# Optimization experiments

Measured on AMD Instinct MI355X. Metric: run time of the kernel, lower is better.

## Reference

```python
import jax, jax.numpy as jnp
import numpy as np

V, D, H, L, B, T = 32000, 1024, 1024, 4, 32, 128
PAD_ID = 0


def setup_inputs() -> dict:
    key = jax.random.key(0)
    ks = jax.random.split(key, 12)
    s = lambda fan: 1.0 / np.sqrt(fan)
    dec_input = jax.random.randint(ks[0], (B, T), 0, V)
    h0 = jax.random.normal(ks[1], (L, B, H), jnp.float32)
    c0 = jax.random.normal(ks[2], (L, B, H), jnp.float32)
    emb = jax.random.normal(ks[3], (V, D), jnp.float32) * 0.02
    emb = emb.at[PAD_ID].set(0.0)
    # all layers have input size H (layer0 input = embedding_dim = H)
    W_ih = jax.random.uniform(ks[4], (L, 4 * H, H), jnp.float32, -s(H), s(H))
    W_hh = jax.random.uniform(ks[5], (L, 4 * H, H), jnp.float32, -s(H), s(H))
    b_ih = jax.random.uniform(ks[6], (L, 4 * H), jnp.float32, -s(H), s(H))
    b_hh = jax.random.uniform(ks[7], (L, 4 * H), jnp.float32, -s(H), s(H))
    cls_W = jax.random.uniform(ks[8], (V, H), jnp.float32, -s(H), s(H))
    cls_b = jax.random.uniform(ks[9], (V,), jnp.float32, -s(H), s(H))
    return {"dec_input": dec_input, "h0": h0, "c0": c0, "emb": emb,
            "W_ih": W_ih, "W_hh": W_hh, "b_ih": b_ih, "b_hh": b_hh,
            "cls_W": cls_W, "cls_b": cls_b}


def _lstm_stack_step(carry, x_t, W_ih, W_hh, b_ih, b_hh):
    # carry: (h [L,B,H], c [L,B,H]); x_t: [B,H]
    h, c = carry
    inp = x_t
    hs, cs = [], []
    n_layers = W_ih.shape[0]
    for l in range(n_layers):
        gates = inp @ W_ih[l].T + h[l] @ W_hh[l].T + b_ih[l] + b_hh[l]
        i_g, f_g, g_g, o_g = jnp.split(gates, 4, axis=-1)
        c_new = jax.nn.sigmoid(f_g) * c[l] + jax.nn.sigmoid(i_g) * jnp.tanh(g_g)
        h_new = jax.nn.sigmoid(o_g) * jnp.tanh(c_new)
        inp = h_new + inp  # residual connection (dropout p=0)
        hs.append(h_new)
        cs.append(c_new)
    return (jnp.stack(hs, 0), jnp.stack(cs, 0)), inp


def reference(dec_input, h0, c0, emb, W_ih, W_hh, b_ih, b_hh, cls_W, cls_b):
    embedded = emb[dec_input]                 # [B,T,D]
    xs = jnp.swapaxes(embedded, 0, 1)         # [T,B,D]

    def step(carry, x_t):
        return _lstm_stack_step(carry, x_t, W_ih, W_hh, b_ih, b_hh)

    (hT, cT), outs = jax.lax.scan(step, (h0, c0), xs)  # outs: [T,B,H]
    outputs = jnp.swapaxes(outs, 0, 1)         # [B,T,H]
    logits = outputs @ cls_W.T + cls_b         # [B,T,V]
    return logits, (hT, cT)
```

## Files before the change

### kernel.cpp

```cpp
#include <hip/hip_runtime.h>
#include <stdint.h>

#define LAYERS 4
#define BATCH  32
#define SEQT   128
#define HID    1024
#define VOCAB  32000

typedef __attribute__((ext_vector_type(8))) short short8;
typedef __attribute__((ext_vector_type(8))) __bf16 bf16x8;
typedef __attribute__((ext_vector_type(4))) float floatx4;

#define CLS_OFF  0ul
#define X_OFF    65536000ul
#define RES_OFF  73924608ul
#define HBT_OFF  107479040ul
#define CF_OFF   141295616ul
#define SYNC_OFF 141819904ul

#define LOGITS_N 131072000ul
#define BH (BATCH * HID)

__device__ __forceinline__ unsigned short f2bf(float f) {
  union { float f; unsigned u; } v; v.f = f;
  unsigned r = v.u + 0x7FFF + ((v.u >> 16) & 1);
  return (unsigned short)(r >> 16);
}
__device__ __forceinline__ float bf2f(unsigned short b) {
  union { unsigned u; float f; } v; v.u = ((unsigned)b) << 16;
  return v.f;
}
__device__ __forceinline__ floatx4 mfma16(short8 a, short8 b, floatx4 c) {
  return __builtin_amdgcn_mfma_f32_16x16x32_bf16(
      __builtin_bit_cast(bf16x8, a), __builtin_bit_cast(bf16x8, b), c, 0, 0, 0);
}
__device__ __forceinline__ short8 cvt8(float4 a, float4 b) {
  short8 r;
  r[0] = (short)f2bf(a.x); r[1] = (short)f2bf(a.y);
  r[2] = (short)f2bf(a.z); r[3] = (short)f2bf(a.w);
  r[4] = (short)f2bf(b.x); r[5] = (short)f2bf(b.y);
  r[6] = (short)f2bf(b.z); r[7] = (short)f2bf(b.w);
  return r;
}


__global__ void k_convert(const float* __restrict__ clsw, unsigned short* __restrict__ oC) {
  const long long NC4 = 8192000LL;
  for (long long i = (long long)blockIdx.x * blockDim.x + threadIdx.x; i < NC4;
       i += (long long)gridDim.x * blockDim.x) {
    float4 v = *(const float4*)(clsw + (i << 2));
    ushort4 o; o.x = f2bf(v.x); o.y = f2bf(v.y); o.z = f2bf(v.z); o.w = f2bf(v.w);
    *(ushort4*)(oC + (i << 2)) = o;
  }
}

__global__ void k_embed(const int* __restrict__ tok, const float* __restrict__ emb,
                        unsigned short* __restrict__ X) {
  const int bt = blockIdx.x;
  const int t = bt >> 5, b = bt & 31;
  const int v = tok[b * SEQT + t];
  const float4* src = (const float4*)(emb + (size_t)v * HID);
  ushort4* dst = (ushort4*)(X + (size_t)bt * HID);
  const int i = threadIdx.x;
  float4 f = src[i];
  ushort4 o; o.x = f2bf(f.x); o.y = f2bf(f.y); o.z = f2bf(f.z); o.w = f2bf(f.w);
  dst[i] = o;
}

__global__ void k_init(const float* __restrict__ h0, const float* __restrict__ c0,
                       unsigned short* __restrict__ HBT, float* __restrict__ CF,
                       unsigned* __restrict__ sync) {
  const int i = blockIdx.x * blockDim.x + threadIdx.x;
  if (i < 4096) sync[i] = 0u;
  if (i < LAYERS * BATCH * HID) {
    HBT[i] = f2bf(h0[i]);
    CF[i] = c0[i];
  }
}


__global__ __launch_bounds__(512, 2) void k_lstm(
    const float* __restrict__ Wih, const float* __restrict__ Whh,
    const float* __restrict__ bih, const float* __restrict__ bhh,
    const unsigned short* __restrict__ X, unsigned short* __restrict__ RES,
    unsigned short* __restrict__ HBT, const float* __restrict__ CF,
    float* __restrict__ out, unsigned* __restrict__ syncp) {
  const int p = blockIdx.x;
  const int l = (p & 7) >> 1;
  const int jj = ((p >> 3) << 1) | (p & 1);
  const int j0 = jj << 4;
  const int tid = threadIdx.x;
  const int q = tid >> 6;
  const int lane = tid & 63;
  const int lo = lane & 15, hi = lane >> 4;
  const int u = tid & 15, b = tid >> 4;

  __shared__ float red[8][32][66];
  __shared__ unsigned mbx, mbh;

  if (tid == 0) { mbx = 0u; mbh = 0u; }

  (void)__hip_atomic_load(syncp + 2048, __ATOMIC_ACQUIRE, __HIP_MEMORY_SCOPE_AGENT);

  const unsigned* fx = syncp + (((l - 1) & 3) * 64 + lane) * 4;
  const unsigned* fh = syncp + (l * 64 + lane) * 4;
  unsigned* fown = syncp + (l * 64 + jj) * 4;

  short8 wx[4][4], wh[4][4];
  {
    const size_t lb = (size_t)l * 4096;
#pragma unroll
    for (int ct = 0; ct < 4; ++ct) {
#pragma unroll
      for (int ks = 0; ks < 4; ++ks) {
        const size_t off = (lb + (size_t)(ct * 1024 + j0 + lo)) * HID
                         + (size_t)q * 128 + ks * 32 + hi * 8;
        float4 a0 = *(const float4*)(Wih + off);
        float4 a1 = *(const float4*)(Wih + off + 4);
        wx[ct][ks] = cvt8(a0, a1);
        float4 b0 = *(const float4*)(Whh + off);
        float4 b1 = *(const float4*)(Whh + off + 4);
        wh[ct][ks] = cvt8(b0, b1);
      }
    }
  }
  float bias_g[4];
#pragma unroll
  for (int g = 0; g < 4; ++g)
    bias_g[g] = bih[l * 4096 + g * 1024 + j0 + u] + bhh[l * 4096 + g * 1024 + j0 + u];
  float c_reg = CF[(size_t)l * BH + (size_t)b * HID + j0 + u];

  __syncthreads();

  for (int t = 0; t < SEQT; ++t) {
    if (q == 0) {
      if (l > 0) {
        for (;;) {
          int ok = (__hip_atomic_load(fx, __ATOMIC_RELAXED, __HIP_MEMORY_SCOPE_AGENT)
                    >= (unsigned)(t + 1));
          if (__all(ok)) break;
          __builtin_amdgcn_s_sleep(1);
        }
      }
      __hip_atomic_store(&mbx, (unsigned)(t + 1),
                         __ATOMIC_RELAXED, __HIP_MEMORY_SCOPE_WORKGROUP);
    } else {
      while (__hip_atomic_load(&mbx, __ATOMIC_RELAXED, __HIP_MEMORY_SCOPE_WORKGROUP)
             < (unsigned)(t + 1))
        __builtin_amdgcn_s_sleep(1);
    }

    const unsigned short* xsrc = (l == 0)
        ? (X + (size_t)t * BH)
        : (RES + ((size_t)(l - 1) * SEQT + t) * BH);

    const unsigned short* px0 = xsrc + (size_t)lo * HID + q * 128 + hi * 8;
    const unsigned short* px1 = px0 + 16 * HID;
    const unsigned short* pxr = xsrc + (size_t)b * HID + j0 + u;

    short8 x0a, x0b, x0c, x0d, x1a, x1b, x1c, x1d;
    unsigned xres;
    asm volatile(
      "global_load_dwordx4 %0, %9,  off\n\t"
      "global_load_dwordx4 %1, %9,  off offset:64\n\t"
      "global_load_dwordx4 %2, %9,  off offset:128\n\t"
      "global_load_dwordx4 %3, %9,  off offset:192\n\t"
      "global_load_dwordx4 %4, %10, off\n\t"
      "global_load_dwordx4 %5, %10, off offset:64\n\t"
      "global_load_dwordx4 %6, %10, off offset:128\n\t"
      "global_load_dwordx4 %7, %10, off offset:192\n\t"
      "global_load_ushort  %8, %11, off\n\t"
      "s_waitcnt vmcnt(0)"
      : "=&v"(x0a), "=&v"(x0b), "=&v"(x0c), "=&v"(x0d),
        "=&v"(x1a), "=&v"(x1b), "=&v"(x1c), "=&v"(x1d), "=&v"(xres)
      : "v"(px0), "v"(px1), "v"(pxr)
      : "memory");

    floatx4 acc[4][2];
#pragma unroll
    for (int ct = 0; ct < 4; ++ct) { acc[ct][0] = {0,0,0,0}; acc[ct][1] = {0,0,0,0}; }
#pragma unroll
    for (int ct = 0; ct < 4; ++ct) {
      acc[ct][0] = mfma16(x0a, wx[ct][0], acc[ct][0]);
      acc[ct][1] = mfma16(x1a, wx[ct][0], acc[ct][1]);
      acc[ct][0] = mfma16(x0b, wx[ct][1], acc[ct][0]);
      acc[ct][1] = mfma16(x1b, wx[ct][1], acc[ct][1]);
      acc[ct][0] = mfma16(x0c, wx[ct][2], acc[ct][0]);
      acc[ct][1] = mfma16(x1c, wx[ct][2], acc[ct][1]);
      acc[ct][0] = mfma16(x0d, wx[ct][3], acc[ct][0]);
      acc[ct][1] = mfma16(x1d, wx[ct][3], acc[ct][1]);
    }

    if (q == 0) {
      if (t > 0) {
        for (;;) {
          int ok = (__hip_atomic_load(fh, __ATOMIC_RELAXED, __HIP_MEMORY_SCOPE_AGENT)
                    >= (unsigned)t);
          if (__all(ok)) break;
          __builtin_amdgcn_s_sleep(1);
        }
      }
      __hip_atomic_store(&mbh, (unsigned)(t + 1),
                         __ATOMIC_RELAXED, __HIP_MEMORY_SCOPE_WORKGROUP);
    } else {
      while (__hip_atomic_load(&mbh, __ATOMIC_RELAXED, __HIP_MEMORY_SCOPE_WORKGROUP)
             < (unsigned)(t + 1))
        __builtin_amdgcn_s_sleep(1);
    }

    const unsigned short* hsrc = HBT + ((size_t)t * LAYERS + l) * BH;
    const unsigned short* ph0 = hsrc + (size_t)lo * HID + q * 128 + hi * 8;
    const unsigned short* ph1 = ph0 + 16 * HID;

    short8 h0a, h0b, h0c, h0d, h1a, h1b, h1c, h1d;
    asm volatile(
      "global_load_dwordx4 %0, %8, off\n\t"
      "global_load_dwordx4 %1, %8, off offset:64\n\t"
      "global_load_dwordx4 %2, %8, off offset:128\n\t"
      "global_load_dwordx4 %3, %8, off offset:192\n\t"
      "global_load_dwordx4 %4, %9, off\n\t"
      "global_load_dwordx4 %5, %9, off offset:64\n\t"
      "global_load_dwordx4 %6, %9, off offset:128\n\t"
      "global_load_dwordx4 %7, %9, off offset:192\n\t"
      "s_waitcnt vmcnt(0)"
      : "=&v"(h0a), "=&v"(h0b), "=&v"(h0c), "=&v"(h0d),
        "=&v"(h1a), "=&v"(h1b), "=&v"(h1c), "=&v"(h1d)
      : "v"(ph0), "v"(ph1)
      : "memory");

#pragma unroll
    for (int ct = 0; ct < 4; ++ct) {
      acc[ct][0] = mfma16(h0a, wh[ct][0], acc[ct][0]);
      acc[ct][1] = mfma16(h1a, wh[ct][0], acc[ct][1]);
      acc[ct][0] = mfma16(h0b, wh[ct][1], acc[ct][0]);
      acc[ct][1] = mfma16(h1b, wh[ct][1], acc[ct][1]);
      acc[ct][0] = mfma16(h0c, wh[ct][2], acc[ct][0]);
      acc[ct][1] = mfma16(h1c, wh[ct][2], acc[ct][1]);
      acc[ct][0] = mfma16(h0d, wh[ct][3], acc[ct][0]);
      acc[ct][1] = mfma16(h1d, wh[ct][3], acc[ct][1]);
    }

#pragma unroll
    for (int ct = 0; ct < 4; ++ct)
#pragma unroll
      for (int rt = 0; rt < 2; ++rt)
#pragma unroll
        for (int r = 0; r < 4; ++r)
          red[q][rt * 16 + hi * 4 + r][ct * 16 + lo] = acc[ct][rt][r];
    __syncthreads();

    float gacc[4] = {0.f, 0.f, 0.f, 0.f};
#pragma unroll
    for (int qq = 0; qq < 8; ++qq)
#pragma unroll
      for (int g = 0; g < 4; ++g)
        gacc[g] += red[qq][b][g * 16 + u];

    const float ig = gacc[0] + bias_g[0];
    const float fg = gacc[1] + bias_g[1];
    const float gg = gacc[2] + bias_g[2];
    const float og = gacc[3] + bias_g[3];
    const float si = 1.f / (1.f + __expf(-ig));
    const float sf = 1.f / (1.f + __expf(-fg));
    const float so = 1.f / (1.f + __expf(-og));
    const float tg = 1.f - 2.f / (__expf(2.f * gg) + 1.f);
    const float cn = sf * c_reg + si * tg;
    const float hn = so * (1.f - 2.f / (__expf(2.f * cn) + 1.f));
    c_reg = cn;

    const float xval = bf2f((unsigned short)xres);
    const unsigned hbf = f2bf(hn);
    const unsigned rbf = f2bf(hn + xval);
    const unsigned hpk = hbf | (((unsigned)__shfl_xor((int)hbf, 1)) << 16);
    const unsigned rpk = rbf | (((unsigned)__shfl_xor((int)rbf, 1)) << 16);

    unsigned short* HBw = HBT + ((size_t)(t + 1) * LAYERS + l) * BH;
    unsigned short* RESw = RES + ((size_t)l * SEQT + t) * BH;
    const size_t hidx = (size_t)b * HID + j0 + u;
    if (!(tid & 1)) {
      __hip_atomic_store((unsigned*)(HBw + hidx), hpk,
                         __ATOMIC_RELAXED, __HIP_MEMORY_SCOPE_AGENT);
      __hip_atomic_store((unsigned*)(RESw + hidx), rpk,
                         __ATOMIC_RELAXED, __HIP_MEMORY_SCOPE_AGENT);
    }
    if (t == SEQT - 1) {
      out[LOGITS_N + (size_t)l * BH + hidx] = hn;
      out[LOGITS_N + 131072ul + (size_t)l * BH + hidx] = cn;
    }

    asm volatile("s_waitcnt vmcnt(0)" ::: "memory");
    __syncthreads();
    if (tid == 0)
      __hip_atomic_store(fown, (unsigned)(t + 1),
                         __ATOMIC_RELAXED, __HIP_MEMORY_SCOPE_AGENT);
  }
}


__global__ __launch_bounds__(256, 2) void k_cls(
    const unsigned short* __restrict__ A, const unsigned short* __restrict__ Bw,
    const float* __restrict__ bias, float* __restrict__ out) {
  __shared__ unsigned short lds_s[2][128 * 64];
  unsigned short* lA = lds_s[0];
  unsigned short* lB = lds_s[1];
  const int ntile = blockIdx.x >> 5;
  const int mtile = blockIdx.x & 31;
  const int m0 = mtile << 7, n0 = ntile << 7;
  const int tid = threadIdx.x;
  const int w = tid >> 6, lane = tid & 63, lo = lane & 15, hi = lane >> 4;
  const int mw = (w >> 1) << 6, nw = (w & 1) << 6;

  floatx4 acc[4][4];
#pragma unroll
  for (int i = 0; i < 4; ++i)
#pragma unroll
    for (int j = 0; j < 4; ++j) acc[i][j] = {0.f, 0.f, 0.f, 0.f};

  for (int k0 = 0; k0 < HID; k0 += 64) {
#pragma unroll
    for (int qq = 0; qq < 4; ++qq) {
      const int e = qq * 256 + tid;
      const int row = e >> 3, c8 = e & 7;
      const int ps = row * 64 + ((c8 ^ (row & 7)) << 3);
      *(short8*)(lA + ps) = *(const short8*)(A  + (size_t)(m0 + row) * HID + k0 + (c8 << 3));
      *(short8*)(lB + ps) = *(const short8*)(Bw + (size_t)(n0 + row) * HID + k0 + (c8 << 3));
    }
    __syncthreads();
#pragma unroll
    for (int kk = 0; kk < 2; ++kk) {
      short8 af[4], bfr[4];
#pragma unroll
      for (int x = 0; x < 4; ++x) {
        const int ra = mw + x * 16 + lo;
        af[x]  = *(const short8*)(lA + ra * 64 + ((((kk << 2) + hi) ^ (ra & 7)) << 3));
        const int rb = nw + x * 16 + lo;
        bfr[x] = *(const short8*)(lB + rb * 64 + ((((kk << 2) + hi) ^ (rb & 7)) << 3));
      }
#pragma unroll
      for (int mi = 0; mi < 4; ++mi)
#pragma unroll
        for (int ni = 0; ni < 4; ++ni)
          acc[mi][ni] = mfma16(af[mi], bfr[ni], acc[mi][ni]);
    }
    __syncthreads();
  }

  float* ldsf = (float*)lds_s;
  const int rl = tid >> 5;
  const int c4 = (tid & 31) << 2;
#pragma unroll
  for (int h = 0; h < 2; ++h) {
    __syncthreads();
    if ((mw >> 6) == h) {
#pragma unroll
      for (int mi = 0; mi < 4; ++mi)
#pragma unroll
        for (int ni = 0; ni < 4; ++ni)
#pragma unroll
          for (int r = 0; r < 4; ++r)
            ldsf[(mi * 16 + hi * 4 + r) * 128 + nw + ni * 16 + lo] = acc[mi][ni][r];
    }
    __syncthreads();
#pragma unroll
    for (int it = 0; it < 8; ++it) {
      const int lr = it * 8 + rl;
      const int ra = m0 + h * 64 + lr;
      const int orow = (ra & 31) * SEQT + (ra >> 5);
      const int v = n0 + c4;
      float4 vv = *(float4*)&ldsf[lr * 128 + c4];
      const float4 bb = *(const float4*)&bias[v];
      vv.x += bb.x; vv.y += bb.y; vv.z += bb.z; vv.w += bb.w;
      *(float4*)&out[(size_t)orow * VOCAB + v] = vv;
    }
  }
}


extern "C" void kernel_launch(void* const* d_in, const int* in_sizes, int n_in,
                              void* d_out, int out_size, void* d_ws, size_t ws_size,
                              hipStream_t stream) {
  (void)in_sizes; (void)n_in; (void)out_size; (void)ws_size;
  const int*   tok  = (const int*)d_in[0];
  const float* h0   = (const float*)d_in[1];
  const float* c0   = (const float*)d_in[2];
  const float* emb  = (const float*)d_in[3];
  const float* wih  = (const float*)d_in[4];
  const float* whh  = (const float*)d_in[5];
  const float* bih  = (const float*)d_in[6];
  const float* bhh  = (const float*)d_in[7];
  const float* clsw = (const float*)d_in[8];
  const float* clsb = (const float*)d_in[9];
  float* out = (float*)d_out;
  char* ws = (char*)d_ws;

  unsigned short* Cls = (unsigned short*)(ws + CLS_OFF);
  unsigned short* X   = (unsigned short*)(ws + X_OFF);
  unsigned short* RES = (unsigned short*)(ws + RES_OFF);
  unsigned short* HBT = (unsigned short*)(ws + HBT_OFF);
  float*          CF  = (float*)(ws + CF_OFF);
  unsigned*       SY  = (unsigned*)(ws + SYNC_OFF);

  hipLaunchKernelGGL(k_convert, dim3(2048), dim3(256), 0, stream, clsw, Cls);
  hipLaunchKernelGGL(k_embed,   dim3(SEQT * BATCH), dim3(256), 0, stream, tok, emb, X);
  hipLaunchKernelGGL(k_init,    dim3(512), dim3(256), 0, stream, h0, c0, HBT, CF, SY);

  {
    const float* a0 = wih; const float* a1 = whh; const float* a2 = bih; const float* a3 = bhh;
    const unsigned short* a4 = X; unsigned short* a5 = RES; unsigned short* a6 = HBT;
    const float* a7 = CF; float* a8 = out; unsigned* a9 = SY;
    void* kargs[] = {&a0, &a1, &a2, &a3, &a4, &a5, &a6, &a7, &a8, &a9};
    hipLaunchCooperativeKernel((void*)k_lstm, dim3(256), dim3(512), kargs, 0, stream);
  }

  hipLaunchKernelGGL(k_cls, dim3(250 * 32), dim3(256), 0, stream,
                     RES + (size_t)3 * SEQT * BATCH * HID, Cls, clsb, out);
}
```

Baseline: 1.291 ms.

## Merge LSTM x/h waits and loads; use direct global-to-LDS loads in classifier

In the recurrent kernel, the two separate spin-waits (input from the layer below and hidden state from the previous step) are merged into a single wait, and the x and h tile loads are issued together with interleaved MFMAs. This removes one sync round and one load-latency exposure per timestep, but gives up overlapping the x-part GEMM with waiting for h. Sync flags are also packed densely instead of strided by 4. The classifier GEMM switches to global_load_lds with a swizzled source address so data goes straight into LDS, and its launch bound rises to 4 blocks per CU.

```diff
diff --git a/kernel.cpp b/kernel.cpp
--- a/kernel.cpp
+++ b/kernel.cpp
@@ -96,15 +96,15 @@
   const int u = tid & 15, b = tid >> 4;
 
   __shared__ float red[8][32][66];
-  __shared__ unsigned mbx, mbh;
-
-  if (tid == 0) { mbx = 0u; mbh = 0u; }
+  __shared__ unsigned mbx;
+
+  if (tid == 0) mbx = 0u;
 
   (void)__hip_atomic_load(syncp + 2048, __ATOMIC_ACQUIRE, __HIP_MEMORY_SCOPE_AGENT);
 
-  const unsigned* fx = syncp + (((l - 1) & 3) * 64 + lane) * 4;
-  const unsigned* fh = syncp + (l * 64 + lane) * 4;
-  unsigned* fown = syncp + (l * 64 + jj) * 4;
+  const unsigned* fx = syncp + ((l - 1) & 3) * 64 + lane;
+  const unsigned* fh = syncp + l * 64 + lane;
+  unsigned* fown = syncp + l * 64 + jj;
 
   short8 wx[4][4], wh[4][4];
   {
@@ -134,10 +134,15 @@
 
   for (int t = 0; t < SEQT; ++t) {
     if (q == 0) {
-      if (l > 0) {
+      if (l > 0 || t > 0) {
         for (;;) {
-          int ok = (__hip_atomic_load(fx, __ATOMIC_RELAXED, __HIP_MEMORY_SCOPE_AGENT)
-                    >= (unsigned)(t + 1));
+          int ok = 1;
+          if (l > 0)
+            ok &= (__hip_atomic_load(fx, __ATOMIC_RELAXED, __HIP_MEMORY_SCOPE_AGENT)
+                   >= (unsigned)(t + 1));
+          if (t > 0)
+            ok &= (__hip_atomic_load(fh, __ATOMIC_RELAXED, __HIP_MEMORY_SCOPE_AGENT)
+                   >= (unsigned)t);
           if (__all(ok)) break;
           __builtin_amdgcn_s_sleep(1);
         }
@@ -153,27 +158,42 @@
     const unsigned short* xsrc = (l == 0)
         ? (X + (size_t)t * BH)
         : (RES + ((size_t)(l - 1) * SEQT + t) * BH);
+    const unsigned short* hsrc = HBT + ((size_t)t * LAYERS + l) * BH;
 
     const unsigned short* px0 = xsrc + (size_t)lo * HID + q * 128 + hi * 8;
     const unsigned short* px1 = px0 + 16 * HID;
+    const unsigned short* ph0 = hsrc + (size_t)lo * HID + q * 128 + hi * 8;
+    const unsigned short* ph1 = ph0 + 16 * HID;
     const unsigned short* pxr = xsrc + (size_t)b * HID + j0 + u;
 
     short8 x0a, x0b, x0c, x0d, x1a, x1b, x1c, x1d;
+    short8 h0a, h0b, h0c, h0d, h1a, h1b, h1c, h1d;
     unsigned xres;
     asm volatile(
-      "global_load_dwordx4 %0, %9,  off\n\t"
-      "global_load_dwordx4 %1, %9,  off offset:64\n\t"
-      "global_load_dwordx4 %2, %9,  off offset:128\n\t"
-      "global_load_dwordx4 %3, %9,  off offset:192\n\t"
-      "global_load_dwordx4 %4, %10, off\n\t"
-      "global_load_dwordx4 %5, %10, off offset:64\n\t"
-      "global_load_dwordx4 %6, %10, off offset:128\n\t"
-      "global_load_dwordx4 %7, %10, off offset:192\n\t"
-      "global_load_ushort  %8, %11, off\n\t"
+      "global_load_dwordx4 %0,  %17, off\n\t"
+      "global_load_dwordx4 %1,  %17, off offset:64\n\t"
+      "global_load_dwordx4 %2,  %17, off offset:128\n\t"
+      "global_load_dwordx4 %3,  %17, off offset:192\n\t"
+      "global_load_dwordx4 %4,  %18, off\n\t"
+      "global_load_dwordx4 %5,  %18, off offset:64\n\t"
+      "global_load_dwordx4 %6,  %18, off offset:128\n\t"
+      "global_load_dwordx4 %7,  %18, off offset:192\n\t"
+      "global_load_dwordx4 %8,  %19, off\n\t"
+      "global_load_dwordx4 %9,  %19, off offset:64\n\t"
+      "global_load_dwordx4 %10, %19, off offset:128\n\t"
+      "global_load_dwordx4 %11, %19, off offset:192\n\t"
+      "global_load_dwordx4 %12, %20, off\n\t"
+      "global_load_dwordx4 %13, %20, off offset:64\n\t"
+      "global_load_dwordx4 %14, %20, off offset:128\n\t"
+      "global_load_dwordx4 %15, %20, off offset:192\n\t"
+      "global_load_ushort  %16, %21, off\n\t"
       "s_waitcnt vmcnt(0)"
       : "=&v"(x0a), "=&v"(x0b), "=&v"(x0c), "=&v"(x0d),
-        "=&v"(x1a), "=&v"(x1b), "=&v"(x1c), "=&v"(x1d), "=&v"(xres)
-      : "v"(px0), "v"(px1), "v"(pxr)
+        "=&v"(x1a), "=&v"(x1b), "=&v"(x1c), "=&v"(x1d),
+        "=&v"(h0a), "=&v"(h0b), "=&v"(h0c), "=&v"(h0d),
+        "=&v"(h1a), "=&v"(h1b), "=&v"(h1c), "=&v"(h1d),
+        "=&v"(xres)
+      : "v"(px0), "v"(px1), "v"(ph0), "v"(ph1), "v"(pxr)
       : "memory");
 
     floatx4 acc[4][2];
@@ -183,59 +203,18 @@
     for (int ct = 0; ct < 4; ++ct) {
       acc[ct][0] = mfma16(x0a, wx[ct][0], acc[ct][0]);
       acc[ct][1] = mfma16(x1a, wx[ct][0], acc[ct][1]);
+      acc[ct][0] = mfma16(h0a, wh[ct][0], acc[ct][0]);
+      acc[ct][1] = mfma16(h1a, wh[ct][0], acc[ct][1]);
       acc[ct][0] = mfma16(x0b, wx[ct][1], acc[ct][0]);
       acc[ct][1] = mfma16(x1b, wx[ct][1], acc[ct][1]);
+      acc[ct][0] = mfma16(h0b, wh[ct][1], acc[ct][0]);
+      acc[ct][1] = mfma16(h1b, wh[ct][1], acc[ct][1]);
       acc[ct][0] = mfma16(x0c, wx[ct][2], acc[ct][0]);
       acc[ct][1] = mfma16(x1c, wx[ct][2], acc[ct][1]);
+      acc[ct][0] = mfma16(h0c, wh[ct][2], acc[ct][0]);
+      acc[ct][1] = mfma16(h1c, wh[ct][2], acc[ct][1]);
       acc[ct][0] = mfma16(x0d, wx[ct][3], acc[ct][0]);
       acc[ct][1] = mfma16(x1d, wx[ct][3], acc[ct][1]);
-    }
-
-    if (q == 0) {
-      if (t > 0) {
-        for (;;) {
-          int ok = (__hip_atomic_load(fh, __ATOMIC_RELAXED, __HIP_MEMORY_SCOPE_AGENT)
-                    >= (unsigned)t);
-          if (__all(ok)) break;
-          __builtin_amdgcn_s_sleep(1);
-        }
-      }
-      __hip_atomic_store(&mbh, (unsigned)(t + 1),
-                         __ATOMIC_RELAXED, __HIP_MEMORY_SCOPE_WORKGROUP);
-    } else {
-      while (__hip_atomic_load(&mbh, __ATOMIC_RELAXED, __HIP_MEMORY_SCOPE_WORKGROUP)
-             < (unsigned)(t + 1))
-        __builtin_amdgcn_s_sleep(1);
-    }
-
-    const unsigned short* hsrc = HBT + ((size_t)t * LAYERS + l) * BH;
-    const unsigned short* ph0 = hsrc + (size_t)lo * HID + q * 128 + hi * 8;
-    const unsigned short* ph1 = ph0 + 16 * HID;
-
-    short8 h0a, h0b, h0c, h0d, h1a, h1b, h1c, h1d;
-    asm volatile(
-      "global_load_dwordx4 %0, %8, off\n\t"
-      "global_load_dwordx4 %1, %8, off offset:64\n\t"
-      "global_load_dwordx4 %2, %8, off offset:128\n\t"
-      "global_load_dwordx4 %3, %8, off offset:192\n\t"
-      "global_load_dwordx4 %4, %9, off\n\t"
-      "global_load_dwordx4 %5, %9, off offset:64\n\t"
-      "global_load_dwordx4 %6, %9, off offset:128\n\t"
-      "global_load_dwordx4 %7, %9, off offset:192\n\t"
-      "s_waitcnt vmcnt(0)"
-      : "=&v"(h0a), "=&v"(h0b), "=&v"(h0c), "=&v"(h0d),
-        "=&v"(h1a), "=&v"(h1b), "=&v"(h1c), "=&v"(h1d)
-      : "v"(ph0), "v"(ph1)
-      : "memory");
-
-#pragma unroll
-    for (int ct = 0; ct < 4; ++ct) {
-      acc[ct][0] = mfma16(h0a, wh[ct][0], acc[ct][0]);
-      acc[ct][1] = mfma16(h1a, wh[ct][0], acc[ct][1]);
-      acc[ct][0] = mfma16(h0b, wh[ct][1], acc[ct][0]);
-      acc[ct][1] = mfma16(h1b, wh[ct][1], acc[ct][1]);
-      acc[ct][0] = mfma16(h0c, wh[ct][2], acc[ct][0]);
-      acc[ct][1] = mfma16(h1c, wh[ct][2], acc[ct][1]);
       acc[ct][0] = mfma16(h0d, wh[ct][3], acc[ct][0]);
       acc[ct][1] = mfma16(h1d, wh[ct][3], acc[ct][1]);
     }
@@ -297,7 +276,7 @@
 }
 
 
-__global__ __launch_bounds__(256, 2) void k_cls(
+__global__ __launch_bounds__(256, 4) void k_cls(
     const unsigned short* __restrict__ A, const unsigned short* __restrict__ Bw,
     const float* __restrict__ bias, float* __restrict__ out) {
   __shared__ unsigned short lds_s[2][128 * 64];
@@ -309,6 +288,7 @@
   const int tid = threadIdx.x;
   const int w = tid >> 6, lane = tid & 63, lo = lane & 15, hi = lane >> 4;
   const int mw = (w >> 1) << 6, nw = (w & 1) << 6;
+  const int wbase = (w << 6) << 3;
 
   floatx4 acc[4][4];
 #pragma unroll
@@ -321,9 +301,17 @@
     for (int qq = 0; qq < 4; ++qq) {
       const int e = qq * 256 + tid;
       const int row = e >> 3, c8 = e & 7;
-      const int ps = row * 64 + ((c8 ^ (row & 7)) << 3);
-      *(short8*)(lA + ps) = *(const short8*)(A  + (size_t)(m0 + row) * HID + k0 + (c8 << 3));
-      *(short8*)(lB + ps) = *(const short8*)(Bw + (size_t)(n0 + row) * HID + k0 + (c8 << 3));
+      const int cs = (c8 ^ (row & 7)) << 3;
+      const unsigned short* ga = A  + (size_t)(m0 + row) * HID + k0 + cs;
+      const unsigned short* gb = Bw + (size_t)(n0 + row) * HID + k0 + cs;
+      unsigned short* la = lA + qq * 2048 + wbase;
+      unsigned short* lb = lB + qq * 2048 + wbase;
+      __builtin_amdgcn_global_load_lds(
+          (const __attribute__((address_space(1))) unsigned*)(const void*)ga,
+          (__attribute__((address_space(3))) unsigned*)(void*)la, 16, 0, 0);
+      __builtin_amdgcn_global_load_lds(
+          (const __attribute__((address_space(1))) unsigned*)(const void*)gb,
+          (__attribute__((address_space(3))) unsigned*)(void*)lb, 16, 0, 0);
     }
     __syncthreads();
 #pragma unroll
```

New measurement: 1.526 ms. 18.2% more time.
